# Performance work log

Hardware: AMD Instinct MI355X
Metric: run time of the kernel (lower is better)

Reference implementation:

```python
import jax, jax.numpy as jnp
import numpy as np

S, B, F = 2048, 16, 100
E, H, NOUT, DEC, FF, NH = 512, 512, 10, 1024, 2048, 8
DH = E // NH


def _ln(h, g, b):
    m = h.mean(-1, keepdims=True)
    v = ((h - m) ** 2).mean(-1, keepdims=True)
    return (h - m) * jax.lax.rsqrt(v + 1e-5) * g + b


def setup_inputs() -> dict:
    key = jax.random.key(0)
    ks = jax.random.split(key, 24)
    w = lambda k, shp, s=0.02: (jax.random.normal(k, shp, dtype=jnp.float32) * s)
    return {
        "x": jax.random.normal(ks[0], (S, B, F), dtype=jnp.float32),
        "y": jax.random.normal(ks[1], (S, B), dtype=jnp.float32),
        "enc_W": w(ks[2], (F, E), 0.1), "enc_b": jnp.zeros((E,), jnp.float32),
        "yenc_W": w(ks[3], (1, E), 0.1), "yenc_b": jnp.zeros((E,), jnp.float32),
        "Wq": w(ks[4], (E, E)), "Wk": w(ks[5], (E, E)),
        "Wv": w(ks[6], (E, E)), "Wo": w(ks[7], (E, E)),
        "ln1_g": jnp.ones((E,), jnp.float32), "ln1_b": jnp.zeros((E,), jnp.float32),
        "ln2_g": jnp.ones((E,), jnp.float32), "ln2_b": jnp.zeros((E,), jnp.float32),
        "ffn_W1": w(ks[8], (E, FF)), "ffn_b1": jnp.zeros((FF,), jnp.float32),
        "ffn_W2": w(ks[9], (FF, E)), "ffn_b2": jnp.zeros((E,), jnp.float32),
        "dec_W": w(ks[10], (E, DEC)), "dec_b": jnp.zeros((DEC,), jnp.float32),
        "head_w1_W": w(ks[11], (DEC, F * H)),
        "head_b1_W": w(ks[12], (DEC, H)),
        "head_w2_W": w(ks[13], (DEC, H * NOUT)),
        "head_b2_W": w(ks[14], (DEC, NOUT)),
        "single_eval_pos": 1024,
    }


def reference(x, y, enc_W, enc_b, yenc_W, yenc_b, Wq, Wk, Wv, Wo,
              ln1_g, ln1_b, ln2_g, ln2_b, ffn_W1, ffn_b1, ffn_W2, ffn_b2,
              dec_W, dec_b, head_w1_W, head_b1_W, head_w2_W, head_b2_W,
              single_eval_pos):
    sep = int(single_eval_pos)
    # encoders
    x_src = x @ enc_W + enc_b                       # [S,B,E]
    y_src = y[..., None] @ yenc_W + yenc_b          # [S,B,E]
    train_x = x_src[:sep] + y_src[:sep]             # [T,B,E]

    # inner_forward: one post-LN transformer encoder layer over train tokens
    q = (train_x @ Wq).reshape(sep, B, NH, DH)
    k = (train_x @ Wk).reshape(sep, B, NH, DH)
    v = (train_x @ Wv).reshape(sep, B, NH, DH)
    scores = jnp.einsum('tbhd,sbhd->bhts', q, k) / np.sqrt(DH).astype(np.float32)
    attn = jax.nn.softmax(scores, axis=-1)
    ao = jnp.einsum('bhts,sbhd->tbhd', attn, v).reshape(sep, B, E) @ Wo
    z = _ln(train_x + ao, ln1_g, ln1_b)
    ff = jax.nn.relu(z @ ffn_W1 + ffn_b1) @ ffn_W2 + ffn_b2
    out = _ln(z + ff, ln2_g, ln2_b)                 # [T,B,E]

    # decoder: mean-pool over train tokens, emit per-batch MLP weights
    pooled = out.mean(0)                            # [B,E]
    dh = jax.nn.relu(pooled @ dec_W + dec_b)        # [B,DEC]
    w1 = (dh @ head_w1_W).reshape(B, F, H)
    b1 = dh @ head_b1_W                             # [B,H]
    w2 = (dh @ head_w2_W).reshape(B, H, NOUT)
    b2 = dh @ head_b2_W                             # [B,NOUT]

    # per-batch generated MLP on eval tokens (no_double_embedding path)
    x_eval = jnp.nan_to_num(x[sep:])                # [Eval,B,F]
    h = jnp.einsum('ebf,bfh->ebh', x_eval, w1) + b1
    h = jax.nn.relu(h)
    h = jnp.einsum('ebh,bho->ebo', h, w2) + b2
    return h                                        # [Eval,B,NOUT]
```

## Files before the change

### kernel.cpp

```cpp
#include <hip/hip_runtime.h>
#include <math.h>

#define SEP   1024
#define EVALN 1024
#define BB    16
#define FIN   100
#define FINP  128
#define EE    512
#define NHH   8
#define DHH   64
#define FFNN  2048
#define DECN  1024
#define HHN   512
#define NOUTN 10
#define TBR   (SEP * BB)
#define MB    (1024u * 1024u)

typedef short  s16x8 __attribute__((ext_vector_type(8)));
typedef float  f32x4 __attribute__((ext_vector_type(4)));

__device__ __forceinline__ unsigned short f2b(float f) {
  union { float f; unsigned int u; } v; v.f = f;
  unsigned int u = v.u;
  return (unsigned short)((u + 0x7fffu + ((u >> 16) & 1u)) >> 16);
}

__device__ __forceinline__ float nan2num(float v) {
  if (isnan(v)) return 0.f;
  if (isinf(v)) return v > 0.f ? 3.4028234663852886e38f : -3.4028234663852886e38f;
  return v;
}

__device__ __forceinline__ void gld16(const void* g, void* l) {
  __builtin_amdgcn_global_load_lds(
      (const __attribute__((address_space(1))) unsigned int*)g,
      (__attribute__((address_space(3))) unsigned int*)l, 16, 0, 0);
}

__global__ __launch_bounds__(256)
void prep_fused(const float* __restrict__ x,
                const float* __restrict__ enc_W, const float* __restrict__ Wq,
                const float* __restrict__ Wk, const float* __restrict__ Wv,
                const float* __restrict__ Wo, const float* __restrict__ W1,
                const float* __restrict__ W2,
                unsigned short* __restrict__ xb, unsigned short* __restrict__ WencT,
                unsigned short* __restrict__ WqkvT, unsigned short* __restrict__ WoT,
                unsigned short* __restrict__ W1T, unsigned short* __restrict__ W2T) {
  const int bid = blockIdx.x;
  const int tid = threadIdx.x;
  if (bid < 8192) {
    const int idx = bid * 256 + tid;
    const int m = idx >> 7, f = idx & 127;
    xb[idx] = (f < FIN) ? f2b(x[(size_t)m * FIN + f]) : (unsigned short)0;
    return;
  }
  int t = bid - 8192;
  const float* W; unsigned short* Wt; int K, N, Kp, gx;
  if (t < 64) {
    W = enc_W; Wt = WencT; K = FIN; N = EE; Kp = FINP; gx = 16;
  } else if ((t -= 64) < 256) {
    W = Wq; Wt = WqkvT; K = EE; N = EE; Kp = EE; gx = 16;
  } else if ((t -= 256) < 256) {
    W = Wk; Wt = WqkvT + (size_t)EE * EE; K = EE; N = EE; Kp = EE; gx = 16;
  } else if ((t -= 256) < 256) {
    W = Wv; Wt = WqkvT + (size_t)2 * EE * EE; K = EE; N = EE; Kp = EE; gx = 16;
  } else if ((t -= 256) < 256) {
    W = Wo; Wt = WoT; K = EE; N = EE; Kp = EE; gx = 16;
  } else if ((t -= 256) < 1024) {
    W = W1; Wt = W1T; K = EE; N = FFNN; Kp = EE; gx = 64;
  } else {
    t -= 1024;
    W = W2; Wt = W2T; K = FFNN; N = EE; Kp = FFNN; gx = 16;
  }
  __shared__ float tb[32][33];
  const int n0 = (t % gx) * 32, k0 = (t / gx) * 32;
  const int tx = tid & 31, ty = tid >> 5;
#pragma unroll
  for (int r = 0; r < 4; ++r) {
    const int k = k0 + ty + r * 8;
    tb[ty + r * 8][tx] = (k < K) ? W[(size_t)k * N + n0 + tx] : 0.f;
  }
  __syncthreads();
#pragma unroll
  for (int r = 0; r < 4; ++r) {
    const int n = n0 + ty + r * 8;
    Wt[(size_t)n * Kp + k0 + tx] = f2b(tb[tx][ty + r * 8]);
  }
}

template <bool YENC, bool BIAS, bool RELU, bool OF32, bool OB16>
__global__ __launch_bounds__(256)
void gemm_bf16(const unsigned short* __restrict__ A,
               const unsigned short* __restrict__ Bt,
               float* __restrict__ C32, unsigned short* __restrict__ C16,
               const float* __restrict__ bias, const float* __restrict__ yb2,
               const float* __restrict__ yvec, const float* __restrict__ yW,
               int M, int N, int K) {
  __shared__ unsigned short As[128 * 32];
  __shared__ unsigned short Bs[128 * 32];
  const int tid = threadIdx.x;
  const int wave = tid >> 6, lane = tid & 63;
  const int q = lane >> 4, c = lane & 15;
  const int wm = wave >> 1, wn = wave & 1;
  const int m0 = blockIdx.y * 128, n0 = blockIdx.x * 128;
  const int srow = lane >> 2;
  const int qlog = (lane & 3) ^ (lane >> 4);
  const int rA0 = wave * 32 + srow;
  const int rA1 = rA0 + 16;
  unsigned short* lA0 = As + wave * 1024;
  unsigned short* lA1 = As + wave * 1024 + 512;
  unsigned short* lB0 = Bs + wave * 1024;
  unsigned short* lB1 = Bs + wave * 1024 + 512;
  const unsigned short* gA0 = A + (size_t)(m0 + rA0) * K + qlog * 8;
  const unsigned short* gA1 = A + (size_t)(m0 + rA1) * K + qlog * 8;
  const unsigned short* gB0 = Bt + (size_t)(n0 + rA0) * K + qlog * 8;
  const unsigned short* gB1 = Bt + (size_t)(n0 + rA1) * K + qlog * 8;

  f32x4 acc[4][4];
#pragma unroll
  for (int i = 0; i < 4; ++i)
#pragma unroll
    for (int j = 0; j < 4; ++j) acc[i][j] = (f32x4){0.f, 0.f, 0.f, 0.f};

  const int pchunk = (q ^ (c >> 2)) * 8;
  const int aoff = (wm * 64 + c) * 32 + pchunk;
  const int boff = (wn * 64 + c) * 32 + pchunk;

  for (int k0 = 0; k0 < K; k0 += 32) {
    gld16(gA0 + k0, lA0);
    gld16(gA1 + k0, lA1);
    gld16(gB0 + k0, lB0);
    gld16(gB1 + k0, lB1);
    __syncthreads();
    s16x8 af[4], bf[4];
#pragma unroll
    for (int mi = 0; mi < 4; ++mi)
      af[mi] = *(const s16x8*)&As[aoff + mi * 16 * 32];
#pragma unroll
    for (int ni = 0; ni < 4; ++ni)
      bf[ni] = *(const s16x8*)&Bs[boff + ni * 16 * 32];
#pragma unroll
    for (int mi = 0; mi < 4; ++mi)
#pragma unroll
      for (int ni = 0; ni < 4; ++ni)
        acc[mi][ni] = __builtin_amdgcn_mfma_f32_16x16x32_bf16(
            af[mi], bf[ni], acc[mi][ni], 0, 0, 0);
    __syncthreads();
  }

  float bb[4], yw[4];
#pragma unroll
  for (int ni = 0; ni < 4; ++ni) {
    const int n = n0 + wn * 64 + ni * 16 + c;
    float t = 0.f;
    if (BIAS) t = bias[n];
    if (YENC) t = bias[n] + yb2[n];
    bb[ni] = t;
    yw[ni] = YENC ? yW[n] : 0.f;
  }
#pragma unroll
  for (int mi = 0; mi < 4; ++mi) {
#pragma unroll
    for (int r = 0; r < 4; ++r) {
      const int m = m0 + wm * 64 + mi * 16 + q * 4 + r;
      const float yv = YENC ? yvec[m] : 0.f;
#pragma unroll
      for (int ni = 0; ni < 4; ++ni) {
        const int n = n0 + wn * 64 + ni * 16 + c;
        float val = acc[mi][ni][r] + bb[ni];
        if (YENC) val = fmaf(yv, yw[ni], val);
        if (RELU) val = fmaxf(val, 0.f);
        if (OF32) C32[(size_t)m * N + n] = val;
        if (OB16) C16[(size_t)m * N + n] = f2b(val);
      }
    }
  }
}

__global__ __launch_bounds__(256)
void vtrans(const unsigned short* __restrict__ qkv, unsigned short* __restrict__ vt) {
  __shared__ unsigned short t[64][72];
  const int s0 = blockIdx.x * 64;
  const int h = blockIdx.y, b = blockIdx.z;
  const int tid = threadIdx.x;
  const int r = tid >> 2, o = (tid & 3) * 16;
  const unsigned short* g =
      qkv + ((size_t)(s0 + r) * BB + b) * 1536 + 1024 + h * 64 + o;
  unsigned short tmp[16];
  *(uint4*)tmp = *(const uint4*)g;
  *(uint4*)(tmp + 8) = *(const uint4*)(g + 8);
#pragma unroll
  for (int i = 0; i < 16; ++i) t[o + i][r] = tmp[i];
  __syncthreads();
  unsigned short tmp2[16];
#pragma unroll
  for (int i = 0; i < 16; ++i) {
    const int p = o + i;
    tmp2[i] = t[r][16 * (p & 3) + (p >> 2)];
  }
  unsigned short* out =
      vt + ((size_t)(b * NHH + h) * 64 + r) * 1024 + s0 + o;
  *(uint4*)out = *(const uint4*)&tmp2[0];
  *(uint4*)(out + 8) = *(const uint4*)&tmp2[8];
}

__global__ __launch_bounds__(256)
void attn_mfma(const unsigned short* __restrict__ qkv,
               const unsigned short* __restrict__ vt,
               unsigned short* __restrict__ aob) {
  __shared__ unsigned short Qs[64][72];
  __shared__ unsigned short Ks[64][72];
  __shared__ unsigned short Vts[64][72];
  __shared__ unsigned short Pls[4][16][72];
  const int tid = threadIdx.x;
  const int w = tid >> 6, lane = tid & 63;
  const int q = lane >> 4, c = lane & 15;
  const int hb = blockIdx.x;
  const int h = hb & (NHH - 1), b = hb >> 3;
  const int t0 = blockIdx.y * 64;
  const int bh = b * NHH + h;
  const int sr = tid >> 2, so = (tid & 3) * 16;

  {
    const unsigned short* g =
        qkv + ((size_t)(t0 + sr) * BB + b) * 1536 + h * 64 + so;
    *(uint4*)&Qs[sr][so] = *(const uint4*)g;
    *(uint4*)&Qs[sr][so + 8] = *(const uint4*)(g + 8);
  }
  __syncthreads();
  s16x8 aq[2];
  aq[0] = *(const s16x8*)&Qs[w * 16 + c][q * 8];
  aq[1] = *(const s16x8*)&Qs[w * 16 + c][32 + q * 8];

  float m_s[4], l_s[4];
  f32x4 oacc[4];
#pragma unroll
  for (int r = 0; r < 4; ++r) { m_s[r] = -3.0e38f; l_s[r] = 0.f; }
#pragma unroll
  for (int dt = 0; dt < 4; ++dt) oacc[dt] = (f32x4){0.f, 0.f, 0.f, 0.f};

  uint4 kr0, kr1, vr0, vr1;
  {
    const unsigned short* gk =
        qkv + ((size_t)sr * BB + b) * 1536 + 512 + h * 64 + so;
    kr0 = *(const uint4*)gk; kr1 = *(const uint4*)(gk + 8);
    const unsigned short* gv = vt + ((size_t)bh * 64 + sr) * 1024 + so;
    vr0 = *(const uint4*)gv; vr1 = *(const uint4*)(gv + 8);
  }
  *(uint4*)&Ks[sr][so] = kr0; *(uint4*)&Ks[sr][so + 8] = kr1;
  *(uint4*)&Vts[sr][so] = vr0; *(uint4*)&Vts[sr][so + 8] = vr1;
  __syncthreads();

  for (int s0 = 0; s0 < SEP; s0 += 64) {
    const bool more = (s0 + 64 < SEP);
    if (more) {
      const unsigned short* gk =
          qkv + ((size_t)(s0 + 64 + sr) * BB + b) * 1536 + 512 + h * 64 + so;
      kr0 = *(const uint4*)gk; kr1 = *(const uint4*)(gk + 8);
      const unsigned short* gv =
          vt + ((size_t)bh * 64 + sr) * 1024 + s0 + 64 + so;
      vr0 = *(const uint4*)gv; vr1 = *(const uint4*)(gv + 8);
    }
    f32x4 sacc[4];
#pragma unroll
    for (int ch = 0; ch < 4; ++ch) sacc[ch] = (f32x4){0.f, 0.f, 0.f, 0.f};
    __builtin_amdgcn_s_setprio(1);
#pragma unroll
    for (int ch = 0; ch < 4; ++ch) {
#pragma unroll
      for (int kh = 0; kh < 2; ++kh) {
        s16x8 bk = *(const s16x8*)&Ks[ch * 16 + c][kh * 32 + q * 8];
        sacc[ch] = __builtin_amdgcn_mfma_f32_16x16x32_bf16(
            aq[kh], bk, sacc[ch], 0, 0, 0);
      }
    }
    __builtin_amdgcn_s_setprio(0);
    float rmax[4];
#pragma unroll
    for (int r = 0; r < 4; ++r) {
      float mx = -3.0e38f;
#pragma unroll
      for (int ch = 0; ch < 4; ++ch) mx = fmaxf(mx, sacc[ch][r] * 0.125f);
      rmax[r] = mx;
    }
#pragma unroll
    for (int mask = 1; mask < 16; mask <<= 1)
#pragma unroll
      for (int r = 0; r < 4; ++r)
        rmax[r] = fmaxf(rmax[r], __shfl_xor(rmax[r], mask));
    float alpha[4], rsum[4];
    float p[4][4];
#pragma unroll
    for (int r = 0; r < 4; ++r) {
      const float mnew = fmaxf(m_s[r], rmax[r]);
      alpha[r] = __expf(m_s[r] - mnew);
      float sum = 0.f;
#pragma unroll
      for (int ch = 0; ch < 4; ++ch) {
        const float pv = __expf(sacc[ch][r] * 0.125f - mnew);
        p[ch][r] = pv;
        sum += pv;
      }
      rsum[r] = sum;
      m_s[r] = mnew;
    }
#pragma unroll
    for (int mask = 1; mask < 16; mask <<= 1)
#pragma unroll
      for (int r = 0; r < 4; ++r) rsum[r] += __shfl_xor(rsum[r], mask);
#pragma unroll
    for (int r = 0; r < 4; ++r) l_s[r] = l_s[r] * alpha[r] + rsum[r];
#pragma unroll
    for (int dt = 0; dt < 4; ++dt)
#pragma unroll
      for (int r = 0; r < 4; ++r) oacc[dt][r] *= alpha[r];
#pragma unroll
    for (int r = 0; r < 4; ++r) {
      uint2 pk;
      pk.x = (unsigned)f2b(p[0][r]) | ((unsigned)f2b(p[1][r]) << 16);
      pk.y = (unsigned)f2b(p[2][r]) | ((unsigned)f2b(p[3][r]) << 16);
      *(uint2*)&Pls[w][q * 4 + r][c * 4] = pk;
    }
    __builtin_amdgcn_s_setprio(1);
#pragma unroll
    for (int kh = 0; kh < 2; ++kh) {
      s16x8 ap = *(const s16x8*)&Pls[w][c][kh * 32 + q * 8];
#pragma unroll
      for (int dt = 0; dt < 4; ++dt) {
        s16x8 bv = *(const s16x8*)&Vts[dt * 16 + c][kh * 32 + q * 8];
        oacc[dt] = __builtin_amdgcn_mfma_f32_16x16x32_bf16(
            ap, bv, oacc[dt], 0, 0, 0);
      }
    }
    __builtin_amdgcn_s_setprio(0);
    __syncthreads();
    if (more) {
      *(uint4*)&Ks[sr][so] = kr0; *(uint4*)&Ks[sr][so + 8] = kr1;
      *(uint4*)&Vts[sr][so] = vr0; *(uint4*)&Vts[sr][so + 8] = vr1;
      __syncthreads();
    }
  }
  float inv[4];
#pragma unroll
  for (int r = 0; r < 4; ++r) inv[r] = 1.f / l_s[r];
#pragma unroll
  for (int dt = 0; dt < 4; ++dt) {
#pragma unroll
    for (int r = 0; r < 4; ++r) {
      const int m = t0 + w * 16 + q * 4 + r;
      aob[((size_t)m * BB + b) * EE + h * 64 + dt * 16 + c] =
          f2b(oacc[dt][r] * inv[r]);
    }
  }
}

template <bool B16>
__global__ __launch_bounds__(256)
void ln_k(const float* __restrict__ a, const float* __restrict__ r_,
          const float* __restrict__ g, const float* __restrict__ be,
          float* __restrict__ o32, unsigned short* __restrict__ o16) {
  __shared__ float ss[4], sqs[4];
  const int row = blockIdx.x;
  const int tid = threadIdx.x;
  const size_t base = (size_t)row * EE;
  const float x0 = a[base + tid] + r_[base + tid];
  const float x1 = a[base + tid + 256] + r_[base + tid + 256];
  float s = x0 + x1;
  float sq = x0 * x0 + x1 * x1;
#pragma unroll
  for (int off = 32; off >= 1; off >>= 1) {
    s += __shfl_xor(s, off);
    sq += __shfl_xor(sq, off);
  }
  const int wid = tid >> 6;
  if ((tid & 63) == 0) { ss[wid] = s; sqs[wid] = sq; }
  __syncthreads();
  s = ss[0] + ss[1] + ss[2] + ss[3];
  sq = sqs[0] + sqs[1] + sqs[2] + sqs[3];
  const float mean = s * (1.f / 512.f);
  const float var = sq * (1.f / 512.f) - mean * mean;
  const float rstd = rsqrtf(fmaxf(var, 0.f) + 1e-5f);
  const float v0 = (x0 - mean) * rstd * g[tid] + be[tid];
  const float v1 = (x1 - mean) * rstd * g[tid + 256] + be[tid + 256];
  o32[base + tid] = v0;
  o32[base + tid + 256] = v1;
  if (B16) {
    o16[base + tid] = f2b(v0);
    o16[base + tid + 256] = f2b(v1);
  }
}

__global__ __launch_bounds__(256)
void pool1(const float* __restrict__ outb, float* __restrict__ pp) {
  const int i = blockIdx.x * 256 + threadIdx.x;
  const int ts = blockIdx.y;
  const float* p = outb + (size_t)ts * 64 * (BB * EE) + i;
  float s0 = 0.f, s1 = 0.f, s2 = 0.f, s3 = 0.f;
  for (int t = 0; t < 64; t += 4) {
    s0 += p[(size_t)(t + 0) * (BB * EE)];
    s1 += p[(size_t)(t + 1) * (BB * EE)];
    s2 += p[(size_t)(t + 2) * (BB * EE)];
    s3 += p[(size_t)(t + 3) * (BB * EE)];
  }
  pp[ts * (BB * EE) + i] = (s0 + s1) + (s2 + s3);
}

__global__ __launch_bounds__(256)
void dec_fused(const float* __restrict__ pp, const float* __restrict__ dW,
               const float* __restrict__ db, float* __restrict__ dh) {
  __shared__ float ps[EE];
  const int b = blockIdx.y;
  const int n = blockIdx.x * 256 + threadIdx.x;
  for (int i = threadIdx.x; i < EE; i += 256) {
    float s = 0.f;
#pragma unroll
    for (int ts = 0; ts < 16; ++ts) s += pp[ts * (BB * EE) + b * EE + i];
    ps[i] = s * (1.f / (float)SEP);
  }
  __syncthreads();
  float a0 = db[n], a1 = 0.f, a2 = 0.f, a3 = 0.f;
  for (int k = 0; k < EE; k += 4) {
    const float4 p4 = *(const float4*)&ps[k];
    a0 = fmaf(p4.x, dW[(size_t)(k + 0) * DECN + n], a0);
    a1 = fmaf(p4.y, dW[(size_t)(k + 1) * DECN + n], a1);
    a2 = fmaf(p4.z, dW[(size_t)(k + 2) * DECN + n], a2);
    a3 = fmaf(p4.w, dW[(size_t)(k + 3) * DECN + n], a3);
  }
  dh[b * DECN + n] = fmaxf((a0 + a1) + (a2 + a3), 0.f);
}

template <int KL>
__global__ __launch_bounds__(256)
void hgemm_split(const float* __restrict__ dh, const float* __restrict__ W,
                 float* __restrict__ part, int N) {
  __shared__ float dhs[16][KL];
  const int tid = threadIdx.x;
  const int n0 = blockIdx.x * 1024;
  const int k0 = blockIdx.y * KL;
  for (int i = tid; i < 16 * (KL / 4); i += 256) {
    const int b = i / (KL / 4), kq = i % (KL / 4);
    *(float4*)&dhs[b][kq * 4] = *(const float4*)&dh[b * DECN + k0 + kq * 4];
  }
  __syncthreads();
  float* pb = part + (size_t)blockIdx.y * 16 * N;
  if ((N & 3) == 0) {
    const int n = n0 + tid * 4;
    if (n + 3 < N) {
      float4 acc[16];
#pragma unroll
      for (int b = 0; b < 16; ++b) acc[b] = (float4){0.f, 0.f, 0.f, 0.f};
      for (int kk = 0; kk < KL; kk += 4) {
        float4 w4[4];
#pragma unroll
        for (int i = 0; i < 4; ++i)
          w4[i] = *(const float4*)&W[(size_t)(k0 + kk + i) * N + n];
#pragma unroll
        for (int b = 0; b < 16; ++b) {
          const float4 d4 = *(const float4*)&dhs[b][kk];
          acc[b].x = fmaf(d4.x, w4[0].x, acc[b].x);
          acc[b].y = fmaf(d4.x, w4[0].y, acc[b].y);
          acc[b].z = fmaf(d4.x, w4[0].z, acc[b].z);
          acc[b].w = fmaf(d4.x, w4[0].w, acc[b].w);
          acc[b].x = fmaf(d4.y, w4[1].x, acc[b].x);
          acc[b].y = fmaf(d4.y, w4[1].y, acc[b].y);
          acc[b].z = fmaf(d4.y, w4[1].z, acc[b].z);
          acc[b].w = fmaf(d4.y, w4[1].w, acc[b].w);
          acc[b].x = fmaf(d4.z, w4[2].x, acc[b].x);
          acc[b].y = fmaf(d4.z, w4[2].y, acc[b].y);
          acc[b].z = fmaf(d4.z, w4[2].z, acc[b].z);
          acc[b].w = fmaf(d4.z, w4[2].w, acc[b].w);
          acc[b].x = fmaf(d4.w, w4[3].x, acc[b].x);
          acc[b].y = fmaf(d4.w, w4[3].y, acc[b].y);
          acc[b].z = fmaf(d4.w, w4[3].z, acc[b].z);
          acc[b].w = fmaf(d4.w, w4[3].w, acc[b].w);
        }
      }
#pragma unroll
      for (int b = 0; b < 16; ++b) *(float4*)&pb[(size_t)b * N + n] = acc[b];
    }
  } else {
    const int n = n0 + tid;
    if (n < N) {
      float acc[16];
#pragma unroll
      for (int b = 0; b < 16; ++b) acc[b] = 0.f;
      for (int kk = 0; kk < KL; ++kk) {
        const float w = W[(size_t)(k0 + kk) * N + n];
#pragma unroll
        for (int b = 0; b < 16; ++b) acc[b] = fmaf(dhs[b][kk], w, acc[b]);
      }
#pragma unroll
      for (int b = 0; b < 16; ++b) pb[(size_t)b * N + n] = acc[b];
    }
  }
}

__global__ __launch_bounds__(256)
void hg_reduce(const float* __restrict__ part, float* __restrict__ out,
               int total, int S) {
  const int i4 = (blockIdx.x * 256 + threadIdx.x) * 4;
  if (i4 >= total) return;
  float4 s = *(const float4*)&part[i4];
  for (int p = 1; p < S; ++p) {
    const float4 v = *(const float4*)&part[(size_t)p * total + i4];
    s.x += v.x; s.y += v.y; s.z += v.z; s.w += v.w;
  }
  *(float4*)&out[i4] = s;
}

__global__ __launch_bounds__(256)
void small_heads(const float* __restrict__ dh, const float* __restrict__ hb1W,
                 const float* __restrict__ hb2W, float* __restrict__ b1g,
                 float* __restrict__ b2g) {
  __shared__ float ds[DECN];
  __shared__ float red2[16][NOUTN];
  const int b = blockIdx.y;
  const int tid = threadIdx.x;
  for (int i = tid; i < DECN; i += 256) ds[i] = dh[b * DECN + i];
  __syncthreads();
  if (blockIdx.x == 0) {
#pragma unroll
    for (int pass = 0; pass < 2; ++pass) {
      const int n = tid + pass * 256;
      float a0 = 0.f, a1 = 0.f, a2 = 0.f, a3 = 0.f;
      for (int k = 0; k < DECN; k += 4) {
        a0 = fmaf(ds[k + 0], hb1W[(size_t)(k + 0) * HHN + n], a0);
        a1 = fmaf(ds[k + 1], hb1W[(size_t)(k + 1) * HHN + n], a1);
        a2 = fmaf(ds[k + 2], hb1W[(size_t)(k + 2) * HHN + n], a2);
        a3 = fmaf(ds[k + 3], hb1W[(size_t)(k + 3) * HHN + n], a3);
      }
      b1g[b * HHN + n] = (a0 + a1) + (a2 + a3);
    }
  } else {
    if (tid < 160) {
      const int o = tid % NOUTN, ks = tid / NOUTN;
      float a0 = 0.f, a1 = 0.f;
      const int kb = ks * 64;
      for (int k = 0; k < 64; k += 2) {
        a0 = fmaf(ds[kb + k + 0], hb2W[(size_t)(kb + k + 0) * NOUTN + o], a0);
        a1 = fmaf(ds[kb + k + 1], hb2W[(size_t)(kb + k + 1) * NOUTN + o], a1);
      }
      red2[ks][o] = a0 + a1;
    }
    __syncthreads();
    if (tid < NOUTN) {
      float s = 0.f;
#pragma unroll
      for (int ks = 0; ks < 16; ++ks) s += red2[ks][tid];
      b2g[b * NOUTN + tid] = s;
    }
  }
}

__global__ __launch_bounds__(256)
void eval_fused(const float* __restrict__ x, const float* __restrict__ w1,
                const float* __restrict__ b1, const float* __restrict__ w2,
                const float* __restrict__ b2, float* __restrict__ outp) {
  __shared__ float xs[8][100];
  __shared__ float w2s[HHN][NOUTN];
  __shared__ float hs[8][516];
  __shared__ float red[2][80];
  const int b = blockIdx.y;
  const int e0 = blockIdx.x << 3;
  const int tid = threadIdx.x;
  for (int i = tid; i < 800; i += 256) {
    const int ee = i / 100, f = i - ee * 100;
    xs[ee][f] = nan2num(x[((size_t)(SEP + e0 + ee) * BB + b) * FIN + f]);
  }
  for (int i = tid; i < HHN * NOUTN; i += 256)
    ((float*)w2s)[i] = w2[(size_t)b * (HHN * NOUTN) + i];
  __syncthreads();
  const float bb0 = b1[b * HHN + tid];
  const float bb1 = b1[b * HHN + tid + 256];
  float a0[8], a1[8];
#pragma unroll
  for (int ee = 0; ee < 8; ++ee) { a0[ee] = 0.f; a1[ee] = 0.f; }
  for (int f = 0; f < FIN; ++f) {
    const float w0 = w1[(size_t)b * (FIN * HHN) + (size_t)f * HHN + tid];
    const float w8 = w1[(size_t)b * (FIN * HHN) + (size_t)f * HHN + tid + 256];
#pragma unroll
    for (int ee = 0; ee < 8; ++ee) {
      a0[ee] = fmaf(xs[ee][f], w0, a0[ee]);
      a1[ee] = fmaf(xs[ee][f], w8, a1[ee]);
    }
  }
#pragma unroll
  for (int ee = 0; ee < 8; ++ee) {
    hs[ee][tid]       = fmaxf(a0[ee] + bb0, 0.f);
    hs[ee][tid + 256] = fmaxf(a1[ee] + bb1, 0.f);
  }
  __syncthreads();
  if (tid < 160) {
    const int o = tid % NOUTN;
    const int ee = (tid / NOUTN) % 8;
    const int ks = tid / 80;
    const float* hp = &hs[ee][ks * 256];
    const float* wp = (const float*)w2s + (size_t)ks * 256 * NOUTN + o;
    float c0 = 0.f, c1 = 0.f, c2 = 0.f, c3 = 0.f;
    for (int k = 0; k < 256; k += 4) {
      c0 = fmaf(hp[k + 0], wp[(k + 0) * NOUTN], c0);
      c1 = fmaf(hp[k + 1], wp[(k + 1) * NOUTN], c1);
      c2 = fmaf(hp[k + 2], wp[(k + 2) * NOUTN], c2);
      c3 = fmaf(hp[k + 3], wp[(k + 3) * NOUTN], c3);
    }
    red[ks][ee * NOUTN + o] = (c0 + c1) + (c2 + c3);
  }
  __syncthreads();
  if (tid < 80) {
    const int o = tid % NOUTN, ee = tid / NOUTN;
    outp[((size_t)(e0 + ee) * BB + b) * NOUTN + o] =
        red[0][tid] + red[1][tid] + b2[b * NOUTN + o];
  }
}

extern "C" void kernel_launch(void* const* d_in, const int* in_sizes, int n_in,
                              void* d_out, int out_size, void* d_ws, size_t ws_size,
                              hipStream_t stream) {
  const float* x      = (const float*)d_in[0];
  const float* y      = (const float*)d_in[1];
  const float* enc_W  = (const float*)d_in[2];
  const float* enc_b  = (const float*)d_in[3];
  const float* yenc_W = (const float*)d_in[4];
  const float* yenc_b = (const float*)d_in[5];
  const float* Wq     = (const float*)d_in[6];
  const float* Wk     = (const float*)d_in[7];
  const float* Wv     = (const float*)d_in[8];
  const float* Wo     = (const float*)d_in[9];
  const float* ln1_g  = (const float*)d_in[10];
  const float* ln1_b  = (const float*)d_in[11];
  const float* ln2_g  = (const float*)d_in[12];
  const float* ln2_b  = (const float*)d_in[13];
  const float* ffn_W1 = (const float*)d_in[14];
  const float* ffn_b1 = (const float*)d_in[15];
  const float* ffn_W2 = (const float*)d_in[16];
  const float* ffn_b2 = (const float*)d_in[17];
  const float* dec_W  = (const float*)d_in[18];
  const float* dec_b  = (const float*)d_in[19];
  const float* hw1    = (const float*)d_in[20];
  const float* hb1    = (const float*)d_in[21];
  const float* hw2    = (const float*)d_in[22];
  const float* hb2    = (const float*)d_in[23];

  char* ws = (char*)d_ws;
  unsigned short* ff1b  = (unsigned short*)(ws + 0 * MB);
  unsigned short* xb    = (unsigned short*)(ws + 0 * MB);
  float*          pp    = (float*)(ws + 0 * MB);
  float*          hgp   = (float*)(ws + 2 * MB);
  unsigned short* txb   = (unsigned short*)(ws + 16 * MB);
  unsigned short* vt    = (unsigned short*)(ws + 32 * MB);
  unsigned short* aob   = (unsigned short*)(ws + 48 * MB);
  unsigned short* qkvb  = (unsigned short*)(ws + 64 * MB);
  float*          z32   = (float*)(ws + 64 * MB);
  unsigned short* zb    = (unsigned short*)(ws + 96 * MB);
  float*          tx32  = (float*)(ws + 112 * MB);
  float*          ff2   = (float*)(ws + 112 * MB);
  float*          aop   = (float*)(ws + 144 * MB);
  float*          outb  = (float*)(ws + 144 * MB);
  size_t wo_ = 176 * (size_t)MB;
  unsigned short* WencT = (unsigned short*)(ws + wo_); wo_ += (size_t)EE * FINP * 2;
  unsigned short* WqkvT = (unsigned short*)(ws + wo_); wo_ += (size_t)3 * EE * EE * 2;
  unsigned short* WoT   = (unsigned short*)(ws + wo_); wo_ += (size_t)EE * EE * 2;
  unsigned short* W1T   = (unsigned short*)(ws + wo_); wo_ += (size_t)FFNN * EE * 2;
  unsigned short* W2T   = (unsigned short*)(ws + wo_); wo_ += (size_t)EE * FFNN * 2;
  float* dh     = (float*)(ws + wo_); wo_ += (size_t)BB * DECN * 4;
  float* w1g    = (float*)(ws + wo_); wo_ += (size_t)BB * FIN * HHN * 4;
  float* b1g    = (float*)(ws + wo_); wo_ += (size_t)BB * HHN * 4;
  float* w2g    = (float*)(ws + wo_); wo_ += (size_t)BB * HHN * NOUTN * 4;
  float* b2g    = (float*)(ws + wo_);
  float* outp = (float*)d_out;

  prep_fused<<<8192 + 64 + 4 * 256 + 1024 + 1024, 256, 0, stream>>>(
      x, enc_W, Wq, Wk, Wv, Wo, ffn_W1, ffn_W2,
      xb, WencT, WqkvT, WoT, W1T, W2T);

  gemm_bf16<true, false, false, true, true><<<dim3(EE / 128, TBR / 128), 256, 0, stream>>>(
      xb, WencT, tx32, txb, enc_b, yenc_b, y, yenc_W, TBR, EE, FINP);
  gemm_bf16<false, false, false, false, true><<<dim3(1536 / 128, TBR / 128), 256, 0, stream>>>(
      txb, WqkvT, nullptr, qkvb, nullptr, nullptr, nullptr, nullptr, TBR, 1536, EE);
  vtrans<<<dim3(SEP / 64, NHH, BB), 256, 0, stream>>>(qkvb, vt);
  attn_mfma<<<dim3(NHH * BB, SEP / 64), 256, 0, stream>>>(qkvb, vt, aob);
  gemm_bf16<false, false, false, true, false><<<dim3(EE / 128, TBR / 128), 256, 0, stream>>>(
      aob, WoT, aop, nullptr, nullptr, nullptr, nullptr, nullptr, TBR, EE, EE);
  ln_k<true><<<TBR, 256, 0, stream>>>(tx32, aop, ln1_g, ln1_b, z32, zb);
  gemm_bf16<false, true, true, false, true><<<dim3(FFNN / 128, TBR / 128), 256, 0, stream>>>(
      zb, W1T, nullptr, ff1b, ffn_b1, nullptr, nullptr, nullptr, TBR, FFNN, EE);
  gemm_bf16<false, true, false, true, false><<<dim3(EE / 128, TBR / 128), 256, 0, stream>>>(
      ff1b, W2T, ff2, nullptr, ffn_b2, nullptr, nullptr, nullptr, TBR, EE, FFNN);
  ln_k<false><<<TBR, 256, 0, stream>>>(z32, ff2, ln2_g, ln2_b, outb, nullptr);
  pool1<<<dim3(32, 16), 256, 0, stream>>>(outb, pp);
  dec_fused<<<dim3(DECN / 256, BB), 256, 0, stream>>>(pp, dec_W, dec_b, dh);
  hgemm_split<128><<<dim3(50, 8), 256, 0, stream>>>(dh, hw1, hgp, FIN * HHN);
  hg_reduce<<<800, 256, 0, stream>>>(hgp, w1g, BB * FIN * HHN, 8);
  hgemm_split<64><<<dim3(5, 16), 256, 0, stream>>>(dh, hw2, hgp, HHN * NOUTN);
  hg_reduce<<<80, 256, 0, stream>>>(hgp, w2g, BB * HHN * NOUTN, 16);
  small_heads<<<dim3(2, BB), 256, 0, stream>>>(dh, hb1, hb2, b1g, b2g);
  eval_fused<<<dim3(EVALN / 8, BB), 256, 0, stream>>>(x, w1g, b1g, w2g, b2g, outp);
}
```

Measured before the change: 852.8 us.

## Double-buffer LDS tiles in bf16 GEMM and raise priority around MFMA

```diff
diff --git a/kernel.cpp b/kernel.cpp
--- a/kernel.cpp
+++ b/kernel.cpp
@@ -15,6 +15,7 @@
 #define NOUTN 10
 #define TBR   (SEP * BB)
 #define MB    (1024u * 1024u)
+
 
 typedef short  s16x8 __attribute__((ext_vector_type(8)));
 typedef float  f32x4 __attribute__((ext_vector_type(4)));
@@ -96,8 +97,8 @@
                const float* __restrict__ bias, const float* __restrict__ yb2,
                const float* __restrict__ yvec, const float* __restrict__ yW,
                int M, int N, int K) {
-  __shared__ unsigned short As[128 * 32];
-  __shared__ unsigned short Bs[128 * 32];
+  __shared__ unsigned short As[2][128 * 32];
+  __shared__ unsigned short Bs[2][128 * 32];
   const int tid = threadIdx.x;
   const int wave = tid >> 6, lane = tid & 63;
   const int q = lane >> 4, c = lane & 15;
@@ -107,10 +108,6 @@
   const int qlog = (lane & 3) ^ (lane >> 4);
   const int rA0 = wave * 32 + srow;
   const int rA1 = rA0 + 16;
-  unsigned short* lA0 = As + wave * 1024;
-  unsigned short* lA1 = As + wave * 1024 + 512;
-  unsigned short* lB0 = Bs + wave * 1024;
-  unsigned short* lB1 = Bs + wave * 1024 + 512;
   const unsigned short* gA0 = A + (size_t)(m0 + rA0) * K + qlog * 8;
   const unsigned short* gA1 = A + (size_t)(m0 + rA1) * K + qlog * 8;
   const unsigned short* gB0 = Bt + (size_t)(n0 + rA0) * K + qlog * 8;
@@ -126,27 +123,45 @@
   const int aoff = (wm * 64 + c) * 32 + pchunk;
   const int boff = (wn * 64 + c) * 32 + pchunk;
 
-  for (int k0 = 0; k0 < K; k0 += 32) {
-    gld16(gA0 + k0, lA0);
-    gld16(gA1 + k0, lA1);
-    gld16(gB0 + k0, lB0);
-    gld16(gB1 + k0, lB1);
+#define STAGE(B_, KK)                                 \
+  do {                                                \
+    gld16(gA0 + (KK), &As[B_][wave * 1024]);          \
+    gld16(gA1 + (KK), &As[B_][wave * 1024 + 512]);    \
+    gld16(gB0 + (KK), &Bs[B_][wave * 1024]);          \
+    gld16(gB1 + (KK), &Bs[B_][wave * 1024 + 512]);    \
+  } while (0)
+
+#define COMPUTE(B_)                                                      \
+  do {                                                                   \
+    s16x8 af[4], bf[4];                                                  \
+    _Pragma("unroll")                                                    \
+    for (int mi = 0; mi < 4; ++mi)                                       \
+      af[mi] = *(const s16x8*)&As[B_][aoff + mi * 512];                  \
+    _Pragma("unroll")                                                    \
+    for (int ni = 0; ni < 4; ++ni)                                       \
+      bf[ni] = *(const s16x8*)&Bs[B_][boff + ni * 512];                  \
+    __builtin_amdgcn_s_setprio(1);                                       \
+    _Pragma("unroll")                                                    \
+    for (int mi = 0; mi < 4; ++mi)                                       \
+      _Pragma("unroll")                                                  \
+      for (int ni = 0; ni < 4; ++ni)                                     \
+        acc[mi][ni] = __builtin_amdgcn_mfma_f32_16x16x32_bf16(           \
+            af[mi], bf[ni], acc[mi][ni], 0, 0, 0);                       \
+    __builtin_amdgcn_s_setprio(0);                                       \
+  } while (0)
+
+  STAGE(0, 0);
+  __syncthreads();
+  for (int k0 = 0; k0 + 64 <= K; k0 += 64) {
+    STAGE(1, k0 + 32);
+    COMPUTE(0);
     __syncthreads();
-    s16x8 af[4], bf[4];
-#pragma unroll
-    for (int mi = 0; mi < 4; ++mi)
-      af[mi] = *(const s16x8*)&As[aoff + mi * 16 * 32];
-#pragma unroll
-    for (int ni = 0; ni < 4; ++ni)
-      bf[ni] = *(const s16x8*)&Bs[boff + ni * 16 * 32];
-#pragma unroll
-    for (int mi = 0; mi < 4; ++mi)
-#pragma unroll
-      for (int ni = 0; ni < 4; ++ni)
-        acc[mi][ni] = __builtin_amdgcn_mfma_f32_16x16x32_bf16(
-            af[mi], bf[ni], acc[mi][ni], 0, 0, 0);
+    if (k0 + 64 < K) STAGE(0, k0 + 64);
+    COMPUTE(1);
     __syncthreads();
   }
+#undef STAGE
+#undef COMPUTE
 
   float bb[4], yw[4];
 #pragma unroll
@@ -672,7 +687,6 @@
   prep_fused<<<8192 + 64 + 4 * 256 + 1024 + 1024, 256, 0, stream>>>(
       x, enc_W, Wq, Wk, Wv, Wo, ffn_W1, ffn_W2,
       xb, WencT, WqkvT, WoT, W1T, W2T);
-
   gemm_bf16<true, false, false, true, true><<<dim3(EE / 128, TBR / 128), 256, 0, stream>>>(
       xb, WencT, tx32, txb, enc_b, yenc_b, y, yenc_W, TBR, EE, FINP);
   gemm_bf16<false, false, false, false, true><<<dim3(1536 / 128, TBR / 128), 256, 0, stream>>>(
```

Result: no change. 852.5 us (-0.0%).
